# Performance work log

Measured on AMD Instinct MI355X. Metric: run time of the kernel, lower is better.

Reference implementation:

```python
import jax, jax.numpy as jnp
import numpy as np
import math

B, S, E, H, FF = 8, 1024, 1024, 16, 4096
HD = E // H
N_DOM = 1024          # boolean-domain size used in the custom scale
LN_EPS = 1e-5


def _layernorm(x, g, b, eps=LN_EPS):
    mu = jnp.mean(x, axis=-1, keepdims=True)
    var = jnp.var(x, axis=-1, keepdims=True)
    return (x - mu) * jax.lax.rsqrt(var + eps) * g + b


def setup_inputs() -> dict:
    key = jax.random.key(0)
    ks = jax.random.split(key, 8)
    s_e = 1.0 / math.sqrt(E)
    s_f = 1.0 / math.sqrt(FF)
    return {
        "x": jax.random.normal(ks[0], (B, S, E), jnp.float32),
        "in_proj_w": jax.random.normal(ks[1], (3 * E, E), jnp.float32) * s_e,
        "out_proj_w": jax.random.normal(ks[2], (E, E), jnp.float32) * s_e,
        "ln1_g": jnp.ones((E,), jnp.float32),
        "ln1_b": jnp.zeros((E,), jnp.float32),
        "ln2_g": jnp.ones((E,), jnp.float32),
        "ln2_b": jnp.zeros((E,), jnp.float32),
        "w1": jax.random.normal(ks[3], (FF, E), jnp.float32) * s_e,
        "b1": jax.random.normal(ks[4], (FF,), jnp.float32) * 0.01,
        "w2": jax.random.normal(ks[5], (E, FF), jnp.float32) * s_f,
        "b2": jax.random.normal(ks[6], (E,), jnp.float32) * 0.01,
    }


def reference(x, in_proj_w, out_proj_w, ln1_g, ln1_b, ln2_g, ln2_b, w1, b1, w2, b2):
    # --- custom multi-head attention (bias=False, dropout=0) ---
    qkv = jnp.einsum("bse,fe->bsf", x, in_proj_w)              # [B,S,3E]
    q, k, v = jnp.split(qkv, 3, axis=-1)
    q = q.reshape(B, S, H, HD)
    k = k.reshape(B, S, H, HD)
    v = v.reshape(B, S, H, HD)
    # nonstandard scale: sqrt(1/head_dim) * 2 * log(N)
    scale = math.sqrt(1.0 / HD) * 2.0 * math.log(N_DOM)
    scores = jnp.einsum("bqhd,bkhd->bhqk", q * scale, k)       # [B,H,S,S]
    attn = jax.nn.softmax(scores, axis=-1)
    ctx = jnp.einsum("bhqk,bkhd->bqhd", attn, v).reshape(B, S, E)
    attn_out = jnp.einsum("bse,fe->bsf", ctx, out_proj_w)      # [B,S,E]
    # --- residual + norm + FFN + residual + norm ---
    h = _layernorm(x + attn_out, ln1_g, ln1_b)
    ff = jnp.einsum("bsf,ef->bse", jax.nn.relu(jnp.einsum("bse,fe->bsf", h, w1) + b1), w2) + b2
    return _layernorm(h + ff, ln2_g, ln2_b)
```

## Files before the change

### kernel.cpp

```cpp
#include <hip/hip_runtime.h>
#include <cstdint>
#include <cmath>


typedef _Float16 f16;
typedef _Float16 f16x8 __attribute__((ext_vector_type(8)));
typedef _Float16 f16x4 __attribute__((ext_vector_type(4)));
typedef __bf16   bf16;
typedef __bf16   bf16x8 __attribute__((ext_vector_type(8)));
typedef __bf16   bf16x4 __attribute__((ext_vector_type(4)));
typedef __bf16   bf16x2 __attribute__((ext_vector_type(2)));
typedef float    f32x4  __attribute__((ext_vector_type(4)));
typedef float    f32x16 __attribute__((ext_vector_type(16)));
typedef unsigned int uint2v __attribute__((ext_vector_type(2)));
typedef unsigned int u32x4v __attribute__((ext_vector_type(4)));

#define B_SZ  8
#define S_SZ  1024
#define E_SZ  1024
#define H_SZ  16
#define HD_SZ 64
#define FF_SZ 4096
#define MTOK  (B_SZ * S_SZ)

__device__ __forceinline__ void async_ld16(const void* g, void* l) {
  __builtin_amdgcn_global_load_lds(
      (const __attribute__((address_space(1))) void*)(uintptr_t)g,
      (__attribute__((address_space(3))) void*)(uint32_t)(uintptr_t)l,
      16, 0, 0);
}

__device__ __forceinline__ void permswap(uint32_t& a, uint32_t& b) {
  uint2v r = __builtin_amdgcn_permlane32_swap(a, b, false, false);
  a = r[0];
  b = r[1];
}

__global__ void cast_kernel(const float* __restrict__ in, f16* __restrict__ out, int n4) {
  int i = blockIdx.x * blockDim.x + threadIdx.x;
  if (i < n4) {
    float4 f = ((const float4*)in)[i];
    f16x4 o = {(f16)f.x, (f16)f.y, (f16)f.z, (f16)f.w};
    ((f16x4*)out)[i] = o;
  }
}

template <bool OUT_F16, bool RELU>
__global__ void gemm_bt(const f16* __restrict__ A, const f16* __restrict__ Bm,
                        const float* __restrict__ bias, void* __restrict__ Cp,
                        int M, int N, int K, int bf16_from_bn) {
  __shared__ f16 As[128 * 64];
  __shared__ f16 Bs[128 * 64];

  const int tid  = threadIdx.x;
  const int wave = tid >> 6;
  const int lane = tid & 63;
  const int quad = lane >> 4;
  const int l16  = lane & 15;
  const int c7   = l16 & 7;
  const int wr   = wave >> 1;
  const int wc   = wave & 1;
  const int bm   = blockIdx.y;
  const int bn   = blockIdx.x;

  f32x4 acc[4][4];
#pragma unroll
  for (int i = 0; i < 4; i++)
#pragma unroll
    for (int j = 0; j < 4; j++) acc[i][j] = (f32x4){0.f, 0.f, 0.f, 0.f};

  const int rii  = wave * 8 + (lane >> 3);
  const int soct = (lane & 7) ^ (rii & 7);
  const f16* gA = A + ((size_t)bm * 128 + rii) * (size_t)K + soct * 8;
  const f16* gB = Bm + ((size_t)bn * 128 + rii) * (size_t)K + soct * 8;

  for (int k0 = 0; k0 < K; k0 += 64) {
    __syncthreads();
#pragma unroll
    for (int i = 0; i < 4; i++)
      async_ld16(gA + (size_t)i * 32 * K + k0, &As[(i * 32 + wave * 8) * 64]);
#pragma unroll
    for (int i = 0; i < 4; i++)
      async_ld16(gB + (size_t)i * 32 * K + k0, &Bs[(i * 32 + wave * 8) * 64]);
    __syncthreads();

#pragma unroll
    for (int kd2 = 0; kd2 < 2; kd2++) {
      f16x8 af[4], bfv[4];
#pragma unroll
      for (int mi = 0; mi < 4; mi++)
        af[mi] = *(const f16x8*)&As[(wr * 64 + mi * 16 + l16) * 64 + (((kd2 * 4 + quad) ^ c7) << 3)];
#pragma unroll
      for (int ni = 0; ni < 4; ni++)
        bfv[ni] = *(const f16x8*)&Bs[(wc * 64 + ni * 16 + l16) * 64 + (((kd2 * 4 + quad) ^ c7) << 3)];
#pragma unroll
      for (int mi = 0; mi < 4; mi++)
#pragma unroll
        for (int ni = 0; ni < 4; ni++)
          acc[mi][ni] = __builtin_amdgcn_mfma_f32_16x16x32_f16(af[mi], bfv[ni], acc[mi][ni], 0, 0, 0);
    }
  }

  const int rowBase = bm * 128 + wr * 64;
  const int colBase = bn * 128 + wc * 64;
  const bool store_bf16 = OUT_F16 && (bn >= bf16_from_bn);
#pragma unroll
  for (int ni = 0; ni < 4; ni++) {
    const int col = colBase + ni * 16 + l16;
    const float bv = (bias != nullptr) ? bias[col] : 0.f;
#pragma unroll
    for (int mi = 0; mi < 4; mi++) {
#pragma unroll
      for (int r = 0; r < 4; r++) {
        const int row = rowBase + mi * 16 + quad * 4 + r;
        float v = acc[mi][ni][r] + bv;
        if (RELU) v = fmaxf(v, 0.f);
        if (OUT_F16) {
          if (store_bf16)
            ((bf16*)Cp)[(size_t)row * N + col] = (bf16)v;
          else
            ((f16*)Cp)[(size_t)row * N + col] = (f16)v;
        } else {
          ((float*)Cp)[(size_t)row * N + col] = v;
        }
      }
    }
  }
}

__global__ __launch_bounds__(256, 4)
void attn_kernel(const f16* __restrict__ qkv, f16* __restrict__ ctx,
                 float scale2, float c2) {
  __shared__ __align__(16) char pool[33280];
  f16*  Ks = (f16*)pool;
  bf16* Vt = (bf16*)(pool + 16384);

  const int tid  = threadIdx.x;
  const int wave = tid >> 6;
  const int lane = tid & 63;
  const int l31  = lane & 31;
  const int hi   = lane >> 5;

  const int flat = blockIdx.x;
  const int bh   = flat & 127;
  const int qt   = flat >> 7;
  const int b    = bh >> 4;
  const int h    = bh & 15;

  const int rs = 3 * E_SZ;
  const size_t tokbase = (size_t)b * S_SZ;

  const int su  = lane >> 3;
  const int soc = (lane & 7) ^ su;

  {
    const f16* gq = qkv + (tokbase + qt * 128 + wave * 8 + su) * (size_t)rs + h * HD_SZ + soc * 8;
#pragma unroll
    for (int i = 0; i < 4; i++)
      async_ld16(gq + (size_t)i * 32 * rs, pool + (i * 32 + wave * 8) * 128);
  }
  __syncthreads();

  f16x8 aq[4];
  {
    const int qrow = wave * 32 + l31;
#pragma unroll
    for (int ks = 0; ks < 4; ks++)
      aq[ks] = *(const f16x8*)&Ks[qrow * 64 + (((ks * 2 + hi) ^ (qrow & 7)) << 3)];
  }

  float Lp = 0.f;
  f32x16 oacc[2];
#pragma unroll
  for (int nb = 0; nb < 2; nb++)
#pragma unroll
    for (int i = 0; i < 16; i++) oacc[nb][i] = 0.f;

  const int vc  = (tid & 7) * 8;
  const int vk0 = (tid >> 3) * 4;

  for (int t = 0; t < S_SZ / 128; t++) {
    __syncthreads();
    {
      const f16* gk = qkv + (tokbase + t * 128 + wave * 8 + su) * (size_t)rs + E_SZ + h * HD_SZ + soc * 8;
#pragma unroll
      for (int i = 0; i < 4; i++)
        async_ld16(gk + (size_t)i * 32 * rs, pool + (i * 32 + wave * 8) * 128);
    }
    {
      const bf16* gv = (const bf16*)qkv + (tokbase + t * 128 + vk0) * (size_t)rs + 2 * E_SZ + h * HD_SZ + vc;
      bf16x8 v0 = *(const bf16x8*)(gv);
      bf16x8 v1 = *(const bf16x8*)(gv + rs);
      bf16x8 v2 = *(const bf16x8*)(gv + 2 * rs);
      bf16x8 v3 = *(const bf16x8*)(gv + 3 * rs);
#pragma unroll
      for (int e = 0; e < 8; e++) {
        bf16x4 pk = {v0[e], v1[e], v2[e], v3[e]};
        *(bf16x4*)&Vt[(vc + e) * 132 + vk0] = pk;
      }
    }
    __syncthreads();

#pragma unroll
    for (int nt = 0; nt < 4; nt++) {
      f32x16 sacc;
#pragma unroll
      for (int i = 0; i < 16; i++) sacc[i] = 0.f;

      const int krow = nt * 32 + l31;
      __builtin_amdgcn_s_setprio(1);
#pragma unroll
      for (int ks = 0; ks < 4; ks++) {
        f16x8 kf = *(const f16x8*)&Ks[krow * 64 + (((ks * 2 + hi) ^ (krow & 7)) << 3)];
        sacc = __builtin_amdgcn_mfma_f32_32x32x16_f16(kf, aq[ks], sacc, 0, 0, 0);
      }
      __builtin_amdgcn_s_setprio(0);

      uint32_t w[8];
#pragma unroll
      for (int j = 0; j < 8; j++) {
        float p0 = exp2f(fmaf(sacc[2 * j],     scale2, -c2));
        float p1 = exp2f(fmaf(sacc[2 * j + 1], scale2, -c2));
        Lp += p0 + p1;
        bf16x2 pk2 = {(bf16)p0, (bf16)p1};
        w[j] = __builtin_bit_cast(uint32_t, pk2);
      }
      permswap(w[0], w[2]);
      permswap(w[1], w[3]);
      permswap(w[4], w[6]);
      permswap(w[5], w[7]);
      u32x4v pe = {w[0], w[1], w[2], w[3]};
      u32x4v po = {w[4], w[5], w[6], w[7]};
      bf16x8 pa[2] = {__builtin_bit_cast(bf16x8, pe), __builtin_bit_cast(bf16x8, po)};

      __builtin_amdgcn_s_setprio(1);
#pragma unroll
      for (int nb = 0; nb < 2; nb++) {
        const int d = nb * 32 + l31;
#pragma unroll
        for (int kst = 0; kst < 2; kst++) {
          const int key = (nt * 2 + kst) * 16 + hi * 8;
          bf16x4 blo = *(const bf16x4*)&Vt[d * 132 + key];
          bf16x4 bhi = *(const bf16x4*)&Vt[d * 132 + key + 4];
          bf16x8 bv = __builtin_shufflevector(blo, bhi, 0, 1, 2, 3, 4, 5, 6, 7);
          oacc[nb] = __builtin_amdgcn_mfma_f32_32x32x16_bf16(pa[kst], bv, oacc[nb], 0, 0, 0);
        }
      }
      __builtin_amdgcn_s_setprio(0);
    }
  }

  float Lfull = Lp + __shfl_xor(Lp, 32, 64);
  const float inv = 1.f / Lfull;
#pragma unroll
  for (int r = 0; r < 16; r++) {
    const int qrow = (r & 3) + 8 * (r >> 2) + 4 * hi;
    const float invr = __shfl(inv, qrow, 32);
    const size_t row = tokbase + (size_t)qt * 128 + wave * 32 + qrow;
#pragma unroll
    for (int nb = 0; nb < 2; nb++)
      ctx[row * (size_t)E_SZ + h * HD_SZ + nb * 32 + l31] = (f16)(oacc[nb][r] * invr);
  }
}

__global__ void ln_kernel(const float* __restrict__ a, const float* __restrict__ res,
                          const float* __restrict__ g, const float* __restrict__ bta,
                          float* __restrict__ out32, f16* __restrict__ out16) {
  const int row  = blockIdx.x;
  const int tid  = threadIdx.x;
  const int wave = tid >> 6;
  const int lane = tid & 63;
  const size_t base = (size_t)row * 1024;
  const int c = tid * 4;

  float4 va = *(const float4*)&a[base + c];
  float4 vr = *(const float4*)&res[base + c];
  float v0 = va.x + vr.x, v1 = va.y + vr.y, v2 = va.z + vr.z, v3 = va.w + vr.w;

  __shared__ float r1[4], r2[4];
  float s = v0 + v1 + v2 + v3;
#pragma unroll
  for (int off = 32; off; off >>= 1) s += __shfl_xor(s, off, 64);
  if (lane == 0) r1[wave] = s;
  __syncthreads();
  const float mu = (r1[0] + r1[1] + r1[2] + r1[3]) * (1.f / 1024.f);

  float d0 = v0 - mu, d1 = v1 - mu, d2 = v2 - mu, d3 = v3 - mu;
  float ss = d0 * d0 + d1 * d1 + d2 * d2 + d3 * d3;
#pragma unroll
  for (int off = 32; off; off >>= 1) ss += __shfl_xor(ss, off, 64);
  if (lane == 0) r2[wave] = ss;
  __syncthreads();
  const float var = (r2[0] + r2[1] + r2[2] + r2[3]) * (1.f / 1024.f);
  const float rsq = rsqrtf(var + 1e-5f);

  float4 gg = *(const float4*)&g[c];
  float4 bb = *(const float4*)&bta[c];
  float o0 = d0 * rsq * gg.x + bb.x;
  float o1 = d1 * rsq * gg.y + bb.y;
  float o2 = d2 * rsq * gg.z + bb.z;
  float o3 = d3 * rsq * gg.w + bb.w;
  float4 o = {o0, o1, o2, o3};
  *(float4*)&out32[base + c] = o;
  if (out16 != nullptr) {
    f16x4 ob = {(f16)o0, (f16)o1, (f16)o2, (f16)o3};
    *(f16x4*)&out16[base + c] = ob;
  }
}

extern "C" void kernel_launch(void* const* d_in, const int* in_sizes, int n_in,
                              void* d_out, int out_size, void* d_ws, size_t ws_size,
                              hipStream_t stream) {
  const float* x    = (const float*)d_in[0];
  const float* wqkv = (const float*)d_in[1];
  const float* wo   = (const float*)d_in[2];
  const float* ln1g = (const float*)d_in[3];
  const float* ln1b = (const float*)d_in[4];
  const float* ln2g = (const float*)d_in[5];
  const float* ln2b = (const float*)d_in[6];
  const float* w1   = (const float*)d_in[7];
  const float* b1   = (const float*)d_in[8];
  const float* w2   = (const float*)d_in[9];
  const float* b2   = (const float*)d_in[10];
  float* out = (float*)d_out;

  char* ws = (char*)d_ws;
  f16* w_inb  = (f16*)(ws + 0);
  f16* w_outb = (f16*)(ws + 6291456);
  f16* w1b    = (f16*)(ws + 8388608);
  f16* w2b    = (f16*)(ws + 16777216);
  f16* xb     = (f16*)(ws + 25165824);
  f16* qkv    = (f16*)(ws + 41943040);
  f16* ctx    = (f16*)(ws + 92274688);
  f16* ff1    = (f16*)(ws + 41943040);
  float* tmp  = (float*)(ws + 109051904);
  float* hbuf = (float*)(ws + 142606336);
  f16* hb     = xb;

  const int NOBF = 1 << 30;

  cast_kernel<<<3072, 256, 0, stream>>>(wqkv, w_inb, 3 * E_SZ * E_SZ / 4);
  cast_kernel<<<1024, 256, 0, stream>>>(wo, w_outb, E_SZ * E_SZ / 4);
  cast_kernel<<<4096, 256, 0, stream>>>(w1, w1b, FF_SZ * E_SZ / 4);
  cast_kernel<<<4096, 256, 0, stream>>>(w2, w2b, E_SZ * FF_SZ / 4);
  cast_kernel<<<8192, 256, 0, stream>>>(x, xb, MTOK * E_SZ / 4);

  gemm_bt<true, false><<<dim3(3 * E_SZ / 128, MTOK / 128), 256, 0, stream>>>(
      xb, w_inb, nullptr, qkv, MTOK, 3 * E_SZ, E_SZ, 16);

  attn_kernel<<<1024, 256, 0, stream>>>(qkv, ctx, 2.5f, 60.0f);

  gemm_bt<false, false><<<dim3(E_SZ / 128, MTOK / 128), 256, 0, stream>>>(
      ctx, w_outb, nullptr, tmp, MTOK, E_SZ, E_SZ, NOBF);

  ln_kernel<<<MTOK, 256, 0, stream>>>(tmp, x, ln1g, ln1b, hbuf, hb);

  gemm_bt<true, true><<<dim3(FF_SZ / 128, MTOK / 128), 256, 0, stream>>>(
      hb, w1b, b1, ff1, MTOK, FF_SZ, E_SZ, NOBF);

  gemm_bt<false, false><<<dim3(E_SZ / 128, MTOK / 128), 256, 0, stream>>>(
      ff1, w2b, b2, tmp, MTOK, E_SZ, FF_SZ, NOBF);

  ln_kernel<<<MTOK, 256, 0, stream>>>(tmp, hbuf, ln2g, ln2b, out, nullptr);

  (void)in_sizes; (void)n_in; (void)out_size; (void)ws_size;
}
```

Measured before the change: 493.4 us.

## Replace GEMM with 256-row double-buffered, 8-wave pipelined kernel and XCD-aware block remap

Swaps the 128x128 single-buffered GEMM for a 256xBN tile kernel with 512 threads, double-buffered LDS and async global-to-LDS prefetch of the next K tile, overlapped with the MFMA work. The loop waits on explicit vmcnt, raises wave priority around MFMA blocks, and remaps block IDs across the 8 XCDs for better L2 locality. The aim is to hide global load latency, which the old per-tile syncthreads round trip exposed, and to increase data reuse per tile. The costs are more LDS per block, higher register pressure from 8x4 accumulators, and hand-tuned waitcnt logic that must track the number of outstanding loads exactly.

New measurement: 503.6 us. 2.1% more time.

```diff
diff --git a/kernel.cpp b/kernel.cpp
--- a/kernel.cpp
+++ b/kernel.cpp
@@ -30,6 +30,15 @@
       16, 0, 0);
 }
 
+template <int N>
+__device__ __forceinline__ void wait_vm() {
+  if constexpr (N == 0)      asm volatile("s_waitcnt vmcnt(0)" ::: "memory");
+  else if constexpr (N == 3) asm volatile("s_waitcnt vmcnt(3)" ::: "memory");
+  else if constexpr (N == 4) asm volatile("s_waitcnt vmcnt(4)" ::: "memory");
+  else static_assert(N == 0 || N == 3 || N == 4, "unsupported vmcnt");
+  __builtin_amdgcn_sched_barrier(0);
+}
+
 __device__ __forceinline__ void permswap(uint32_t& a, uint32_t& b) {
   uint2v r = __builtin_amdgcn_permlane32_swap(a, b, false, false);
   a = r[0];
@@ -45,74 +54,150 @@
   }
 }
 
-template <bool OUT_F16, bool RELU>
-__global__ void gemm_bt(const f16* __restrict__ A, const f16* __restrict__ Bm,
-                        const float* __restrict__ bias, void* __restrict__ Cp,
-                        int M, int N, int K, int bf16_from_bn) {
-  __shared__ f16 As[128 * 64];
-  __shared__ f16 Bs[128 * 64];
+template <int BN, bool OUT_F16, bool RELU>
+__global__ __launch_bounds__(512, 2)
+void gemm256(const f16* __restrict__ A, const f16* __restrict__ Bm,
+             const float* __restrict__ bias, void* __restrict__ Cp,
+             int M, int N, int K, int bf16_from_col) {
+  static_assert(BN == 256 || BN == 128, "BN must be 256 or 128");
+  constexpr int NBCH  = (BN == 256) ? 2 : 1;
+  constexpr int CHUNK = 4096;
+  constexpr int NIF   = 2 + NBCH;
+  constexpr int WN    = (BN == 256) ? 4 : 2;
+  constexpr int FM    = (BN == 256) ? 8 : 4;
+
+  __shared__ f16 lds[(8 + 4 * NBCH) * CHUNK];
+  f16* Ab = lds;
+  f16* Bb = lds + 8 * CHUNK;
 
   const int tid  = threadIdx.x;
   const int wave = tid >> 6;
   const int lane = tid & 63;
   const int quad = lane >> 4;
   const int l16  = lane & 15;
-  const int c7   = l16 & 7;
-  const int wr   = wave >> 1;
-  const int wc   = wave & 1;
-  const int bm   = blockIdx.y;
-  const int bn   = blockIdx.x;
-
-  f32x4 acc[4][4];
-#pragma unroll
-  for (int i = 0; i < 4; i++)
-#pragma unroll
-    for (int j = 0; j < 4; j++) acc[i][j] = (f32x4){0.f, 0.f, 0.f, 0.f};
-
-  const int rii  = wave * 8 + (lane >> 3);
-  const int soct = (lane & 7) ^ (rii & 7);
-  const f16* gA = A + ((size_t)bm * 128 + rii) * (size_t)K + soct * 8;
-  const f16* gB = Bm + ((size_t)bn * 128 + rii) * (size_t)K + soct * 8;
-
-  for (int k0 = 0; k0 < K; k0 += 64) {
-    __syncthreads();
-#pragma unroll
-    for (int i = 0; i < 4; i++)
-      async_ld16(gA + (size_t)i * 32 * K + k0, &As[(i * 32 + wave * 8) * 64]);
-#pragma unroll
-    for (int i = 0; i < 4; i++)
-      async_ld16(gB + (size_t)i * 32 * K + k0, &Bs[(i * 32 + wave * 8) * 64]);
-    __syncthreads();
-
-#pragma unroll
-    for (int kd2 = 0; kd2 < 2; kd2++) {
-      f16x8 af[4], bfv[4];
-#pragma unroll
-      for (int mi = 0; mi < 4; mi++)
-        af[mi] = *(const f16x8*)&As[(wr * 64 + mi * 16 + l16) * 64 + (((kd2 * 4 + quad) ^ c7) << 3)];
-#pragma unroll
-      for (int ni = 0; ni < 4; ni++)
-        bfv[ni] = *(const f16x8*)&Bs[(wc * 64 + ni * 16 + l16) * 64 + (((kd2 * 4 + quad) ^ c7) << 3)];
-#pragma unroll
-      for (int mi = 0; mi < 4; mi++)
-#pragma unroll
-        for (int ni = 0; ni < 4; ni++)
-          acc[mi][ni] = __builtin_amdgcn_mfma_f32_16x16x32_f16(af[mi], bfv[ni], acc[mi][ni], 0, 0, 0);
+
+  const int wm  = wave / WN;
+  const int wn  = wave % WN;
+  const int ah  = (BN == 256) ? wm : (wm >> 1);
+  const int amB = (BN == 256) ? 0 : (wm & 1) * 64;
+  const int bh  = (BN == 256) ? (wn >> 1) : 0;
+  const int bnB = (BN == 256) ? (wn & 1) * 64 : wn * 64;
+
+  int logical = blockIdx.x;
+  {
+    const int nwg = gridDim.x;
+    if ((nwg & 7) == 0) logical = (logical & 7) * (nwg >> 3) + (logical >> 3);
+  }
+  const int gx = N / BN;
+  const int bn = logical % gx;
+  const int bm = logical / gx;
+
+  f32x4 acc[FM][4];
+#pragma unroll
+  for (int mi = 0; mi < FM; mi++)
+#pragma unroll
+    for (int ni = 0; ni < 4; ni++) acc[mi][ni] = (f32x4){0.f, 0.f, 0.f, 0.f};
+
+  const int rr_s = tid >> 2;
+  const int lo_s = (tid & 3) ^ ((rr_s >> 1) & 3);
+  const int wofs = wave * 512;
+  const f16* gAb = A  + ((size_t)bm * 256 + rr_s) * (size_t)K + lo_s * 8;
+  const f16* gBb = Bm + ((size_t)bn * BN  + rr_s) * (size_t)K + lo_s * 8;
+
+  auto stA = [&](int bb, int s, int h, int kt) {
+    async_ld16(gAb + (size_t)h * 128 * K + kt * 64 + s * 32,
+               Ab + ((((bb << 1) + s) << 1) + h) * CHUNK + wofs);
+  };
+  auto stB = [&](int bb, int s, int h, int kt) {
+    async_ld16(gBb + (size_t)h * 128 * K + kt * 64 + s * 32,
+               Bb + (((bb << 1) + s) * NBCH + h) * CHUNK + wofs);
+  };
+  auto rdFrag = [&](const f16* ch, int rr) -> f16x8 {
+    return *(const f16x8*)&ch[rr * 32 + ((quad ^ ((rr >> 1) & 3)) << 3)];
+  };
+
+  const int NT = K >> 6;
+
+#pragma unroll
+  for (int s = 0; s < 2; s++) {
+    stA(0, s, 0, 0);
+    stA(0, s, 1, 0);
+    stB(0, s, 0, 0);
+    if constexpr (NBCH == 2) stB(0, s, 1, 0);
+  }
+  wait_vm<NIF>();
+  __builtin_amdgcn_s_barrier();
+
+  for (int t = 0; t < NT; t++) {
+    const int cur = t & 1, oth = cur ^ 1;
+    const bool last = (t == NT - 1);
+#pragma unroll
+    for (int s = 0; s < 2; s++) {
+      if (!last) { stA(oth, s, 0, t + 1); stA(oth, s, 1, t + 1); }
+      const f16* Ach = Ab + ((((cur << 1) + s) << 1) + ah) * CHUNK;
+      const f16* Bch = Bb + (((cur << 1) + s) * NBCH + bh) * CHUNK;
+      f16x8 bfr[4];
+#pragma unroll
+      for (int ni = 0; ni < 4; ni++) bfr[ni] = rdFrag(Bch, bnB + ni * 16 + l16);
+
+      if constexpr (BN == 256) {
+        f16x8 af[4];
+#pragma unroll
+        for (int i = 0; i < 4; i++) af[i] = rdFrag(Ach, amB + i * 16 + l16);
+        __builtin_amdgcn_s_setprio(1);
+#pragma unroll
+        for (int i = 0; i < 4; i++)
+#pragma unroll
+          for (int ni = 0; ni < 4; ni++)
+            acc[i][ni] = __builtin_amdgcn_mfma_f32_16x16x32_f16(af[i], bfr[ni], acc[i][ni], 0, 0, 0);
+        __builtin_amdgcn_s_setprio(0);
+        __builtin_amdgcn_s_barrier();
+        if (!last) { stB(oth, s, 0, t + 1); stB(oth, s, 1, t + 1); }
+#pragma unroll
+        for (int i = 0; i < 4; i++) af[i] = rdFrag(Ach, amB + (4 + i) * 16 + l16);
+        __builtin_amdgcn_s_setprio(1);
+#pragma unroll
+        for (int i = 0; i < 4; i++)
+#pragma unroll
+          for (int ni = 0; ni < 4; ni++)
+            acc[4 + i][ni] = __builtin_amdgcn_mfma_f32_16x16x32_f16(af[i], bfr[ni], acc[4 + i][ni], 0, 0, 0);
+        __builtin_amdgcn_s_setprio(0);
+      } else {
+        if (!last) stB(oth, s, 0, t + 1);
+        f16x8 af[4];
+#pragma unroll
+        for (int i = 0; i < 4; i++) af[i] = rdFrag(Ach, amB + i * 16 + l16);
+        __builtin_amdgcn_s_setprio(1);
+#pragma unroll
+        for (int i = 0; i < 4; i++)
+#pragma unroll
+          for (int ni = 0; ni < 4; ni++)
+            acc[i][ni] = __builtin_amdgcn_mfma_f32_16x16x32_f16(af[i], bfr[ni], acc[i][ni], 0, 0, 0);
+        __builtin_amdgcn_s_setprio(0);
+      }
+
+      if (!last) {
+        wait_vm<NIF>();
+        __builtin_amdgcn_s_barrier();
+      } else if (s == 0) {
+        wait_vm<0>();
+        __builtin_amdgcn_s_barrier();
+      }
     }
   }
 
-  const int rowBase = bm * 128 + wr * 64;
-  const int colBase = bn * 128 + wc * 64;
-  const bool store_bf16 = OUT_F16 && (bn >= bf16_from_bn);
+  const int rowW = bm * 256 + ((BN == 256) ? wm * 128 : wm * 64);
+  const int colW = bn * BN + wn * 64;
+  const bool store_bf16 = OUT_F16 && (bn * BN >= bf16_from_col);
 #pragma unroll
   for (int ni = 0; ni < 4; ni++) {
-    const int col = colBase + ni * 16 + l16;
+    const int col = colW + ni * 16 + l16;
     const float bv = (bias != nullptr) ? bias[col] : 0.f;
 #pragma unroll
-    for (int mi = 0; mi < 4; mi++) {
+    for (int mi = 0; mi < FM; mi++) {
 #pragma unroll
       for (int r = 0; r < 4; r++) {
-        const int row = rowBase + mi * 16 + quad * 4 + r;
+        const int row = rowW + mi * 16 + quad * 4 + r;
         float v = acc[mi][ni][r] + bv;
         if (RELU) v = fmaxf(v, 0.f);
         if (OUT_F16) {
@@ -126,6 +211,7 @@
       }
     }
   }
+  (void)M;
 }
 
 __global__ __launch_bounds__(256, 4)
@@ -345,20 +431,20 @@
   cast_kernel<<<4096, 256, 0, stream>>>(w2, w2b, E_SZ * FF_SZ / 4);
   cast_kernel<<<8192, 256, 0, stream>>>(x, xb, MTOK * E_SZ / 4);
 
-  gemm_bt<true, false><<<dim3(3 * E_SZ / 128, MTOK / 128), 256, 0, stream>>>(
-      xb, w_inb, nullptr, qkv, MTOK, 3 * E_SZ, E_SZ, 16);
+  gemm256<256, true, false><<<(3 * E_SZ / 256) * (MTOK / 256), 512, 0, stream>>>(
+      xb, w_inb, nullptr, qkv, MTOK, 3 * E_SZ, E_SZ, 2048);
 
   attn_kernel<<<1024, 256, 0, stream>>>(qkv, ctx, 2.5f, 60.0f);
 
-  gemm_bt<false, false><<<dim3(E_SZ / 128, MTOK / 128), 256, 0, stream>>>(
+  gemm256<128, false, false><<<(E_SZ / 128) * (MTOK / 256), 512, 0, stream>>>(
       ctx, w_outb, nullptr, tmp, MTOK, E_SZ, E_SZ, NOBF);
 
   ln_kernel<<<MTOK, 256, 0, stream>>>(tmp, x, ln1g, ln1b, hbuf, hb);
 
-  gemm_bt<true, true><<<dim3(FF_SZ / 128, MTOK / 128), 256, 0, stream>>>(
+  gemm256<256, true, true><<<(FF_SZ / 256) * (MTOK / 256), 512, 0, stream>>>(
       hb, w1b, b1, ff1, MTOK, FF_SZ, E_SZ, NOBF);
 
-  gemm_bt<false, false><<<dim3(E_SZ / 128, MTOK / 128), 256, 0, stream>>>(
+  gemm256<128, false, false><<<(E_SZ / 128) * (MTOK / 256), 512, 0, stream>>>(
       ff1, w2b, b2, tmp, MTOK, E_SZ, FF_SZ, NOBF);
 
   ln_kernel<<<MTOK, 256, 0, stream>>>(tmp, hbuf, ln2g, ln2b, out, nullptr);
```
